# Kernel tuning notes

Measured on AMD Instinct MI355X. Metric: run time of the kernel, lower is better.

The kernel has to match this reference:

```python
import jax, jax.numpy as jnp
import numpy as np

B, C, H, W = 4, 192, 128, 128
HEADS, QK_DIM = 6, 192
DH, DW = 16, 16
STEP_H, STEP_W = DH - 2, DW - 2
EPS = 1e-5


def _starts(size, step, win):
    return np.array([min(i, size - win) for i in range(0, size + step - win, step)], dtype=np.int64)

TOPS = _starts(H, STEP_H, DH)   # [NH]
LEFTS = _starts(W, STEP_W, DW)  # [NW]
NH, NW = len(TOPS), len(LEFTS)
N = NH * NW
ROW = TOPS[:, None] + np.arange(DH)   # [NH, DH]
COL = LEFTS[:, None] + np.arange(DW)  # [NW, DW]

# static per-pixel overlap counts (indices are static w.r.t. H, W)
COUNT = np.zeros((H, W), dtype=np.float32)
for t in TOPS:
    for l in LEFTS:
        COUNT[t:t + DH, l:l + DW] += 1.0
COUNT = jnp.asarray(COUNT)


def setup_inputs() -> dict:
    key = jax.random.key(0)
    ks = jax.random.split(key, 4)
    x = jax.random.normal(ks[0], (B, C, H, W), dtype=jnp.float32)
    Wq = jax.random.normal(ks[1], (QK_DIM, C), dtype=jnp.float32) * 0.02
    Wk = jax.random.normal(ks[2], (QK_DIM, C), dtype=jnp.float32) * 0.02
    Wv = jax.random.normal(ks[3], (C, C), dtype=jnp.float32) * 0.02
    ln_gamma = jnp.ones((C,), dtype=jnp.float32)
    ln_beta = jnp.zeros((C,), dtype=jnp.float32)
    return {"x": x, "Wq": Wq, "Wk": Wk, "Wv": Wv, "ln_gamma": ln_gamma, "ln_beta": ln_beta}


def reference(x, Wq, Wk, Wv, ln_gamma, ln_beta):
    # --- local_partition: gather overlapping windows ---
    r = ROW[:, None, :, None]   # [NH,1,DH,1]
    c = COL[None, :, None, :]   # [1,NW,1,DW]
    win = x[:, :, r, c]                               # [B,C,NH,NW,DH,DW]
    lx = win.transpose(0, 2, 3, 4, 5, 1)              # [B,NH,NW,DH,DW,C]
    lx = lx.reshape(B * N, DH * DW, C)                # [(b n),(dh dw),c]

    # --- LayerNorm over channels ---
    mu = jnp.mean(lx, axis=-1, keepdims=True)
    var = jnp.mean((lx - mu) ** 2, axis=-1, keepdims=True)
    lx = (lx - mu) * jax.lax.rsqrt(var + EPS) * ln_gamma + ln_beta

    # --- VanillaAttention ---
    q = jnp.einsum('bsc,qc->bsq', lx, Wq)
    k = jnp.einsum('bsc,qc->bsq', lx, Wk)
    v = jnp.einsum('bsc,vc->bsv', lx, Wv)
    S = DH * DW
    dq = QK_DIM // HEADS
    dv = C // HEADS
    q = q.reshape(B * N, S, HEADS, dq).transpose(0, 2, 1, 3)  # [bn,h,s,d]
    k = k.reshape(B * N, S, HEADS, dq).transpose(0, 2, 1, 3)
    v = v.reshape(B * N, S, HEADS, dv).transpose(0, 2, 1, 3)
    scale = QK_DIM ** (-0.5)
    attn = jnp.einsum('bhsd,bhtd->bhst', q, k) * scale
    attn = jax.nn.softmax(attn, axis=-1)
    out = jnp.einsum('bhst,bhtd->bhsd', attn, v)
    out = out.transpose(0, 2, 1, 3).reshape(B * N, S, C)

    # --- local_reverse: scatter-add + count-normalize ---
    out = out.reshape(B, NH, NW, DH, DW, C).transpose(0, 5, 1, 2, 3, 4)  # [B,C,NH,NW,DH,DW]
    acc = jnp.zeros_like(x).at[:, :, r, c].add(out)
    return acc / COUNT[None, None]
```

## Files before the change

kernel.cpp:

```cpp
#include <hip/hip_runtime.h>
#include <stdint.h>

#define DEV __device__ __forceinline__

typedef unsigned short u16;
typedef unsigned int u32;
typedef u16   u16x8 __attribute__((ext_vector_type(8)));
typedef u32   u32x4 __attribute__((ext_vector_type(4)));
typedef u32   u32x2 __attribute__((ext_vector_type(2)));
typedef u16   u16x2 __attribute__((ext_vector_type(2)));
typedef __bf16 bf16x8v __attribute__((ext_vector_type(8)));
typedef float f32x4 __attribute__((ext_vector_type(4)));

constexpr int NWIN = 81;
constexpr int BN   = 4 * NWIN;
constexpr float EPS = 1e-5f;
constexpr float QSCALE = 0.07216878364870322f * 1.4426950408889634f;

DEV u16 f2bf(float f) {
    unsigned u = __builtin_bit_cast(unsigned, f);
    u += 0x7fffu + ((u >> 16) & 1u);
    return (u16)(u >> 16);
}
DEV float fexp2(float x) {
    return __builtin_amdgcn_exp2f(x);
}
DEV u32 pack_bf16_hu(float lo, float hi) {
    u32 u0 = __builtin_bit_cast(u32, lo) + 0x8000u;
    u32 u1 = __builtin_bit_cast(u32, hi) + 0x8000u;
    return __builtin_amdgcn_perm(u1, u0, 0x07060302u);
}

DEV f32x4 mfma16(bf16x8v a, bf16x8v b, f32x4 c) {
    return __builtin_amdgcn_mfma_f32_16x16x32_bf16(a, b, c, 0, 0, 0);
}

__global__ void wconv(const float* __restrict__ wq, const float* __restrict__ wk,
                      const float* __restrict__ wv, u16* __restrict__ dst) {
    int idx = blockIdx.x * 256 + threadIdx.x;
    const float* src = (idx < 36864) ? wq : (idx < 73728 ? wk : wv);
    int r = (idx < 36864) ? idx : (idx < 73728 ? idx - 36864 : idx - 73728);
    float v = src[r];
    if (idx < 36864) v *= QSCALE;
    dst[idx] = f2bf(v);
}

__launch_bounds__(256, 2)
__global__ void lnqkv_kernel(const float* __restrict__ x, const u16* __restrict__ wbf,
                             const float* __restrict__ gamma, const float* __restrict__ beta,
                             u16* __restrict__ qk_g, u16* __restrict__ vT_g) {
    __shared__ float p1[8][132], p2[8][132];
    __shared__ float gb[384];
    __shared__ float mu_s[128], rs_s[128];
    __shared__ u16 lx[128 * 200];

    const int bh = blockIdx.x;
    const int b = bh >> 7, hrow = bh & 127;
    const int hw0 = hrow * 128;
    const int tid = threadIdx.x;
    const int w4 = tid & 31, cg = tid >> 5;

    if (tid < 192) { gb[tid] = gamma[tid]; gb[192 + tid] = beta[tid]; }

    const float* base = x + (((long)(b * 192 + cg)) * 128 + hrow) * 128 + 4 * w4;
    {
        float4 s1 = {0, 0, 0, 0}, s2 = {0, 0, 0, 0};
        #pragma unroll 4
        for (int c = 0; c < 192; c += 8) {
            float4 v = *(const float4*)(base + (long)c * 16384);
            s1.x += v.x; s1.y += v.y; s1.z += v.z; s1.w += v.w;
            s2.x += v.x * v.x; s2.y += v.y * v.y; s2.z += v.z * v.z; s2.w += v.w * v.w;
        }
        *(float4*)&p1[cg][4 * w4] = s1;
        *(float4*)&p2[cg][4 * w4] = s2;
    }
    __syncthreads();
    if (tid < 128) {
        float a = 0.f, q = 0.f;
        #pragma unroll
        for (int g = 0; g < 8; ++g) { a += p1[g][tid]; q += p2[g][tid]; }
        float mu = a * (1.0f / 192.0f);
        float var = q * (1.0f / 192.0f) - mu * mu;
        mu_s[tid] = mu; rs_s[tid] = rsqrtf(var + EPS);
    }
    __syncthreads();

    {
        float mu0 = mu_s[4 * w4 + 0], rs0 = rs_s[4 * w4 + 0];
        float mu1 = mu_s[4 * w4 + 1], rs1 = rs_s[4 * w4 + 1];
        float mu2 = mu_s[4 * w4 + 2], rs2 = rs_s[4 * w4 + 2];
        float mu3 = mu_s[4 * w4 + 3], rs3 = rs_s[4 * w4 + 3];
        #pragma unroll 4
        for (int c = cg; c < 192; c += 8) {
            float4 v = *(const float4*)(base + (long)(c - cg) * 16384);
            float g = gb[c], be = gb[192 + c];
            lx[(4 * w4 + 0) * 200 + c] = f2bf((v.x - mu0) * rs0 * g + be);
            lx[(4 * w4 + 1) * 200 + c] = f2bf((v.y - mu1) * rs1 * g + be);
            lx[(4 * w4 + 2) * 200 + c] = f2bf((v.z - mu2) * rs2 * g + be);
            lx[(4 * w4 + 3) * 200 + c] = f2bf((v.w - mu3) * rs3 * g + be);
        }
    }
    __syncthreads();

    const int wv_ = tid >> 6, lane = tid & 63;
    const int l15 = lane & 15, g4 = lane >> 4;

    #pragma unroll 1
    for (int job = 0; job < 3; ++job) {
        const u16* wsrc = wbf + job * 36864;
        bf16x8v B[3][6];
        #pragma unroll
        for (int oi = 0; oi < 3; ++oi)
            #pragma unroll
            for (int ks = 0; ks < 6; ++ks)
                B[oi][ks] = *(const bf16x8v*)&wsrc[(16 * (3 * wv_ + oi) + l15) * 192 + 32 * ks + 8 * g4];

        if (job < 2) {
            const int obase = job * 192;
            const long rowb = ((long)b << 14) + hw0;
            #pragma unroll 1
            for (int m = 0; m < 8; ++m) {
                bf16x8v A[6];
                #pragma unroll
                for (int ks = 0; ks < 6; ++ks)
                    A[ks] = *(const bf16x8v*)&lx[(16 * m + l15) * 200 + 32 * ks + 8 * g4];
                f32x4 acc[3] = {};
                #pragma unroll
                for (int ks = 0; ks < 6; ++ks)
                    #pragma unroll
                    for (int oi = 0; oi < 3; ++oi)
                        acc[oi] = mfma16(A[ks], B[oi][ks], acc[oi]);
                #pragma unroll
                for (int oi = 0; oi < 3; ++oi) {
                    const int o = obase + 16 * (3 * wv_ + oi) + l15;
                    #pragma unroll
                    for (int r = 0; r < 4; ++r)
                        qk_g[(rowb + 16 * m + 4 * g4 + r) * 384 + o] = f2bf(acc[oi][r]);
                }
            }
        } else {
            #pragma unroll 1
            for (int m = 0; m < 8; ++m) {
                bf16x8v A[6];
                #pragma unroll
                for (int ks = 0; ks < 6; ++ks)
                    A[ks] = *(const bf16x8v*)&lx[(16 * m + l15) * 200 + 32 * ks + 8 * g4];
                f32x4 acc[3] = {};
                #pragma unroll
                for (int ks = 0; ks < 6; ++ks)
                    #pragma unroll
                    for (int oi = 0; oi < 3; ++oi)
                        acc[oi] = mfma16(B[oi][ks], A[ks], acc[oi]);
                #pragma unroll
                for (int oi = 0; oi < 3; ++oi)
                    #pragma unroll
                    for (int r = 0; r < 4; ++r) {
                        const int o = 16 * (3 * wv_ + oi) + 4 * g4 + r;
                        vT_g[(((long)(b * 192 + o)) << 14) + hw0 + 16 * m + l15] = f2bf(acc[oi][r]);
                    }
            }
        }
    }
}

__launch_bounds__(512, 2)
__global__ void attn_kernel(const u16* __restrict__ qk_g, const u16* __restrict__ vT_g,
                            float* __restrict__ out_win) {
    __shared__ u16 smem[23808];
    u16* Ks = smem;
    u16* Vs = smem + 10240;
    u32* Pw = (u32*)(smem + 18688);

    const int tid = threadIdx.x;
    const int bid = blockIdx.x;
    const int wg = (bid & 7) * 243 + (bid >> 3);
    const int win = wg % BN, h = wg / BN;
    const int b = win / NWIN, wi = win % NWIN;
    const int t0 = 14 * (wi / 9), l0 = 14 * (wi % 9);

    const int lane = tid & 63, wv_ = tid >> 6;
    const int l15 = lane & 15, g4 = lane >> 4;
    u32* pw = Pw + wv_ * 320;

    bf16x8v bq[2];
    #pragma unroll
    for (int nq = 0; nq < 2; ++nq)
        bq[nq] = *(const bf16x8v*)(qk_g
                 + (((long)b << 14) + (t0 + 2 * wv_ + nq) * 128 + l0 + l15) * 384
                 + 32 * h + 8 * g4);

    {
        int s = tid >> 1, hf = tid & 1;
        int p = (t0 + (s >> 4)) * 128 + l0 + (s & 15);
        const u16* src = qk_g + (((long)b << 14) + p) * 384 + 192 + 32 * h + 16 * hf;
        *(u16x8*)&Ks[s * 40 + 16 * hf    ] = *(const u16x8*)(src);
        *(u16x8*)&Ks[s * 40 + 16 * hf + 8] = *(const u16x8*)(src + 8);

        #pragma unroll
        for (int j = 0; j < 8; ++j) {
            int gid = j * 512 + tid;
            int o = gid >> 7, rq = gid & 127, run = rq >> 3, q = rq & 7;
            const u16* vsrc = vT_g + (((long)(b * 192 + 32 * h + o)) << 14)
                              + (t0 + run) * 128 + l0 + 2 * q;
            *(u16x2*)&Vs[o * 264 + run * 16 + 2 * q] = *(const u16x2*)vsrc;
        }
    }
    __syncthreads();

    const u32x4 ONESW = {0x3F803F80u, 0x3F803F80u, 0x3F803F80u, 0x3F803F80u};
    const bf16x8v aones = __builtin_bit_cast(bf16x8v, ONESW);

    f32x4 oacc[2][2] = {};
    f32x4 osum[2] = {};

    #pragma unroll
    for (int hk = 0; hk < 2; ++hk) {
        u32 pkl[2][8][2];
        #pragma unroll
        for (int nq = 0; nq < 2; ++nq) {
            f32x4 sc[8];
            const f32x4 z = {0.f, 0.f, 0.f, 0.f};
            #pragma unroll
            for (int mtl = 0; mtl < 8; ++mtl) {
                bf16x8v a = *(const bf16x8v*)&Ks[(16 * (8 * hk + mtl) + l15) * 40 + 8 * g4];
                sc[mtl] = mfma16(a, bq[nq], z);
            }
            #pragma unroll
            for (int mtl = 0; mtl < 8; ++mtl) {
                float p0 = fexp2(sc[mtl][0]), p1 = fexp2(sc[mtl][1]);
                float p2 = fexp2(sc[mtl][2]), p3 = fexp2(sc[mtl][3]);
                pkl[nq][mtl][0] = pack_bf16_hu(p0, p1);
                pkl[nq][mtl][1] = pack_bf16_hu(p2, p3);
            }
        }
        #pragma unroll
        for (int c32l = 0; c32l < 4; ++c32l) {
            const int c32 = 4 * hk + c32l;
            bf16x8v a0 = *(const bf16x8v*)&Vs[(l15) * 264 + 32 * c32 + 8 * g4];
            bf16x8v a1 = *(const bf16x8v*)&Vs[(16 + l15) * 264 + 32 * c32 + 8 * g4];
            #pragma unroll
            for (int nq = 0; nq < 2; ++nq) {
                u32x2 w0 = { pkl[nq][2 * c32l    ][0], pkl[nq][2 * c32l    ][1] };
                u32x2 w1 = { pkl[nq][2 * c32l + 1][0], pkl[nq][2 * c32l + 1][1] };
                *(u32x2*)&pw[20 * l15 + 2 * g4    ] = w0;
                *(u32x2*)&pw[20 * l15 + 8 + 2 * g4] = w1;
                u32x4 ww = *(const u32x4*)&pw[20 * l15 + 4 * g4];
                bf16x8v bb = __builtin_bit_cast(bf16x8v, ww);
                oacc[0][nq] = mfma16(a0, bb, oacc[0][nq]);
                oacc[1][nq] = mfma16(a1, bb, oacc[1][nq]);
                osum[nq]    = mfma16(aones, bb, osum[nq]);
            }
        }
    }

    float rden[2] = { 1.0f / osum[0][0], 1.0f / osum[1][0] };
    #pragma unroll
    for (int mtv = 0; mtv < 2; ++mtv)
        #pragma unroll
        for (int nq = 0; nq < 2; ++nq)
            #pragma unroll
            for (int r = 0; r < 4; ++r) {
                int c = 32 * h + 16 * mtv + 4 * g4 + r;
                int q = 16 * (2 * wv_ + nq) + l15;
                out_win[((long)win * 192 + c) * 256 + q] = oacc[mtv][nq][r] * rden[nq];
            }
}

__global__ void gather_kernel(const float* __restrict__ out_win, float* __restrict__ out) {
    int idx = blockIdx.x * 256 + threadIdx.x;
    int w = idx & 127, hh = (idx >> 7) & 127;
    int v = idx >> 14; int c = v % 192, b = v / 192;
    int khmin = (hh - 2) / 14; if (khmin < 0) khmin = 0;
    int khmax = hh / 14; if (khmax > 8) khmax = 8;
    int kwmin = (w - 2) / 14; if (kwmin < 0) kwmin = 0;
    int kwmax = w / 14; if (kwmax > 8) kwmax = 8;
    float acc = 0.f; int cnt = 0;
    for (int ih = khmin; ih <= khmax; ++ih)
        for (int iw = kwmin; iw <= kwmax; ++iw) {
            int win = b * NWIN + ih * 9 + iw;
            int s = (hh - 14 * ih) * 16 + (w - 14 * iw);
            acc += out_win[((long)win * 192 + c) * 256 + s];
            ++cnt;
        }
    float rc = (cnt == 1) ? 1.0f : (cnt == 2 ? 0.5f : 0.25f);
    out[idx] = acc * rc;
}

extern "C" void kernel_launch(void* const* d_in, const int* in_sizes, int n_in,
                              void* d_out, int out_size, void* d_ws, size_t ws_size,
                              hipStream_t stream) {
    const float* x     = (const float*)d_in[0];
    const float* Wq    = (const float*)d_in[1];
    const float* Wk    = (const float*)d_in[2];
    const float* Wv    = (const float*)d_in[3];
    const float* gamma = (const float*)d_in[4];
    const float* beta  = (const float*)d_in[5];

    char* ws = (char*)d_ws;
    u16*   wbf     = (u16*)ws;
    u16*   qk_g    = (u16*)(ws + 221184);
    u16*   vT_g    = (u16*)(ws + 221184 + 50331648L);
    float* out_win = (float*)(ws + 221184 + 75497472L);

    wconv<<<dim3(432), dim3(256), 0, stream>>>(Wq, Wk, Wv, wbf);
    lnqkv_kernel<<<dim3(512), dim3(256), 0, stream>>>(x, wbf, gamma, beta, qk_g, vT_g);
    attn_kernel<<<dim3(BN * 6), dim3(512), 0, stream>>>(qk_g, vT_g, out_win);
    gather_kernel<<<dim3(49152), dim3(256), 0, stream>>>(out_win, (float*)d_out);
}
```

Measured before the change: 127.1 us.

## Hold x tile in registers, alias LN scratch into lx, raise occupancy

```diff
diff --git a/kernel.cpp b/kernel.cpp
--- a/kernel.cpp
+++ b/kernel.cpp
@@ -45,14 +45,13 @@
     dst[idx] = f2bf(v);
 }
 
-__launch_bounds__(256, 2)
+__launch_bounds__(256, 3)
 __global__ void lnqkv_kernel(const float* __restrict__ x, const u16* __restrict__ wbf,
                              const float* __restrict__ gamma, const float* __restrict__ beta,
                              u16* __restrict__ qk_g, u16* __restrict__ vT_g) {
-    __shared__ float p1[8][132], p2[8][132];
+    __shared__ __align__(16) u16 lx[128 * 198];
     __shared__ float gb[384];
     __shared__ float mu_s[128], rs_s[128];
-    __shared__ u16 lx[128 * 200];
 
     const int bh = blockIdx.x;
     const int b = bh >> 7, hrow = bh & 127;
@@ -62,23 +61,31 @@
 
     if (tid < 192) { gb[tid] = gamma[tid]; gb[192 + tid] = beta[tid]; }
 
+    float* p1f = (float*)lx;
+    float* p2f = p1f + 1056;
+
     const float* base = x + (((long)(b * 192 + cg)) * 128 + hrow) * 128 + 4 * w4;
+    float4 xr[24];
+    #pragma unroll
+    for (int i = 0; i < 24; ++i)
+        xr[i] = *(const float4*)(base + (long)(8 * i) * 16384);
+
     {
         float4 s1 = {0, 0, 0, 0}, s2 = {0, 0, 0, 0};
-        #pragma unroll 4
-        for (int c = 0; c < 192; c += 8) {
-            float4 v = *(const float4*)(base + (long)c * 16384);
+        #pragma unroll
+        for (int i = 0; i < 24; ++i) {
+            float4 v = xr[i];
             s1.x += v.x; s1.y += v.y; s1.z += v.z; s1.w += v.w;
             s2.x += v.x * v.x; s2.y += v.y * v.y; s2.z += v.z * v.z; s2.w += v.w * v.w;
         }
-        *(float4*)&p1[cg][4 * w4] = s1;
-        *(float4*)&p2[cg][4 * w4] = s2;
+        *(float4*)&p1f[cg * 132 + 4 * w4] = s1;
+        *(float4*)&p2f[cg * 132 + 4 * w4] = s2;
     }
     __syncthreads();
     if (tid < 128) {
         float a = 0.f, q = 0.f;
         #pragma unroll
-        for (int g = 0; g < 8; ++g) { a += p1[g][tid]; q += p2[g][tid]; }
+        for (int g = 0; g < 8; ++g) { a += p1f[g * 132 + tid]; q += p2f[g * 132 + tid]; }
         float mu = a * (1.0f / 192.0f);
         float var = q * (1.0f / 192.0f) - mu * mu;
         mu_s[tid] = mu; rs_s[tid] = rsqrtf(var + EPS);
@@ -90,30 +97,40 @@
         float mu1 = mu_s[4 * w4 + 1], rs1 = rs_s[4 * w4 + 1];
         float mu2 = mu_s[4 * w4 + 2], rs2 = rs_s[4 * w4 + 2];
         float mu3 = mu_s[4 * w4 + 3], rs3 = rs_s[4 * w4 + 3];
-        #pragma unroll 4
-        for (int c = cg; c < 192; c += 8) {
-            float4 v = *(const float4*)(base + (long)(c - cg) * 16384);
+        #pragma unroll
+        for (int i = 0; i < 24; ++i) {
+            const int c = cg + 8 * i;
             float g = gb[c], be = gb[192 + c];
-            lx[(4 * w4 + 0) * 200 + c] = f2bf((v.x - mu0) * rs0 * g + be);
-            lx[(4 * w4 + 1) * 200 + c] = f2bf((v.y - mu1) * rs1 * g + be);
-            lx[(4 * w4 + 2) * 200 + c] = f2bf((v.z - mu2) * rs2 * g + be);
-            lx[(4 * w4 + 3) * 200 + c] = f2bf((v.w - mu3) * rs3 * g + be);
-        }
-    }
-    __syncthreads();
+            float4 v = xr[i];
+            lx[(4 * w4 + 0) * 198 + c] = f2bf((v.x - mu0) * rs0 * g + be);
+            lx[(4 * w4 + 1) * 198 + c] = f2bf((v.y - mu1) * rs1 * g + be);
+            lx[(4 * w4 + 2) * 198 + c] = f2bf((v.z - mu2) * rs2 * g + be);
+            lx[(4 * w4 + 3) * 198 + c] = f2bf((v.w - mu3) * rs3 * g + be);
+        }
+    }
 
     const int wv_ = tid >> 6, lane = tid & 63;
     const int l15 = lane & 15, g4 = lane >> 4;
 
+    bf16x8v B[3][6];
+    #pragma unroll
+    for (int oi = 0; oi < 3; ++oi)
+        #pragma unroll
+        for (int ks = 0; ks < 6; ++ks)
+            B[oi][ks] = *(const bf16x8v*)&wbf[(16 * (3 * wv_ + oi) + l15) * 192 + 32 * ks + 8 * g4];
+
+    __syncthreads();
+
     #pragma unroll 1
     for (int job = 0; job < 3; ++job) {
-        const u16* wsrc = wbf + job * 36864;
-        bf16x8v B[3][6];
-        #pragma unroll
-        for (int oi = 0; oi < 3; ++oi)
-            #pragma unroll
-            for (int ks = 0; ks < 6; ++ks)
-                B[oi][ks] = *(const bf16x8v*)&wsrc[(16 * (3 * wv_ + oi) + l15) * 192 + 32 * ks + 8 * g4];
+        if (job > 0) {
+            const u16* wsrc = wbf + job * 36864;
+            #pragma unroll
+            for (int oi = 0; oi < 3; ++oi)
+                #pragma unroll
+                for (int ks = 0; ks < 6; ++ks)
+                    B[oi][ks] = *(const bf16x8v*)&wsrc[(16 * (3 * wv_ + oi) + l15) * 192 + 32 * ks + 8 * g4];
+        }
 
         if (job < 2) {
             const int obase = job * 192;
@@ -123,7 +140,7 @@
                 bf16x8v A[6];
                 #pragma unroll
                 for (int ks = 0; ks < 6; ++ks)
-                    A[ks] = *(const bf16x8v*)&lx[(16 * m + l15) * 200 + 32 * ks + 8 * g4];
+                    A[ks] = *(const bf16x8v*)&lx[(16 * m + l15) * 198 + 32 * ks + 8 * g4];
                 f32x4 acc[3] = {};
                 #pragma unroll
                 for (int ks = 0; ks < 6; ++ks)
@@ -144,7 +161,7 @@
                 bf16x8v A[6];
                 #pragma unroll
                 for (int ks = 0; ks < 6; ++ks)
-                    A[ks] = *(const bf16x8v*)&lx[(16 * m + l15) * 200 + 32 * ks + 8 * g4];
+                    A[ks] = *(const bf16x8v*)&lx[(16 * m + l15) * 198 + 32 * ks + 8 * g4];
                 f32x4 acc[3] = {};
                 #pragma unroll
                 for (int ks = 0; ks < 6; ++ks)
```

New measurement: 121.0 us. -4.8%, faster.
